# Kernel tuning notes

Measured on AMD Instinct MI355X. Metric: run time of the kernel, lower is better.

## Reference

```python
import jax, jax.numpy as jnp
import numpy as np

H, D = 4, 64          # n_heads, feats_per_head (hidden_size = H*D = 256)
NEG_SLOPE = 0.2       # DGL GATv2Conv default negative_slope

N_GT, N_UBS, N_AG = 100000, 20000, 20000
E_SEEN, E_NEAR = 320000, 160000
F_GT, F_UBS, F_AG = 8, 8, 16
HID = H * D


def _linear_params(key, fan_in, fan_out):
    kw, kb = jax.random.split(key)
    s = 1.0 / np.sqrt(fan_in)
    W = jax.random.uniform(kw, (fan_in, fan_out), jnp.float32, -s, s)
    b = jax.random.uniform(kb, (fan_out,), jnp.float32, -s, s)
    return W, b


def setup_inputs() -> dict:
    key = jax.random.key(0)
    ks = jax.random.split(key, 16)
    inp = {
        'x_gt': jax.random.normal(ks[0], (N_GT, F_GT), jnp.float32),
        'x_ubs': jax.random.normal(ks[1], (N_UBS, F_UBS), jnp.float32),
        'x_agent': jax.random.normal(ks[2], (N_AG, F_AG), jnp.float32),
        'seen_src': jax.random.randint(ks[3], (E_SEEN,), 0, N_GT, jnp.int32),
        'seen_dst': jax.random.randint(ks[4], (E_SEEN,), 0, N_AG, jnp.int32),
        'near_src': jax.random.randint(ks[5], (E_NEAR,), 0, N_UBS, jnp.int32),
        'near_dst': jax.random.randint(ks[6], (E_NEAR,), 0, N_AG, jnp.int32),
    }
    # GATv2Conv 'seen': (gt -> agent)
    inp['Ws_seen'], inp['bs_seen'] = _linear_params(ks[7], F_GT, HID)
    inp['Wd_seen'], inp['bd_seen'] = _linear_params(ks[8], F_AG, HID)
    inp['attn_seen'] = jax.random.normal(ks[9], (H, D), jnp.float32) * 0.1
    inp['Wr_seen'], inp['br_seen'] = _linear_params(ks[10], F_AG, HID)
    # GATv2Conv 'near': (ubs -> agent)
    inp['Ws_near'], inp['bs_near'] = _linear_params(ks[11], F_UBS, HID)
    inp['Wd_near'], inp['bd_near'] = _linear_params(ks[12], F_AG, HID)
    inp['attn_near'] = jax.random.normal(ks[13], (H, D), jnp.float32) * 0.1
    inp['Wr_near'], inp['br_near'] = _linear_params(ks[14], F_AG, HID)
    # aggregation MLP: Linear(2*HID, HID) + ReLU
    inp['W_aggr'], inp['b_aggr'] = _linear_params(ks[15], 2 * HID, HID)
    return inp


def _gatv2(h_src, h_dst, src, dst, Ws, bs, Wd, bd, attn, Wr, br, n_dst):
    # DGL GATv2Conv, bipartite, residual=True, allow_zero_in_degree, ReLU activation
    fs = (h_src @ Ws + bs).reshape(-1, H, D)   # [Ns,H,D]
    fd = (h_dst @ Wd + bd).reshape(-1, H, D)   # [Nd,H,D]
    e = jax.nn.leaky_relu(fs[src] + fd[dst], NEG_SLOPE)     # [E,H,D]
    scores = jnp.einsum('ehd,hd->eh', e, attn)              # [E,H]
    # edge softmax over incoming edges of each dst node
    m = jax.ops.segment_max(scores, dst, num_segments=n_dst)
    m = jnp.where(jnp.isfinite(m), m, 0.0)                  # zero-in-degree guard
    ex = jnp.exp(scores - m[dst])
    denom = jax.ops.segment_sum(ex, dst, num_segments=n_dst)
    alpha = ex / denom[dst]                                 # [E,H]
    rst = jax.ops.segment_sum(alpha[:, :, None] * fs[src], dst, num_segments=n_dst)
    rst = rst + (h_dst @ Wr + br).reshape(-1, H, D)         # residual
    return jax.nn.relu(rst).reshape(n_dst, H * D)


def reference(x_gt, x_ubs, x_agent, seen_src, seen_dst, near_src, near_dst,
              Ws_seen, bs_seen, Wd_seen, bd_seen, attn_seen, Wr_seen, br_seen,
              Ws_near, bs_near, Wd_near, bd_near, attn_near, Wr_near, br_near,
              W_aggr, b_aggr):
    n_ag = x_agent.shape[0]
    x1 = _gatv2(x_gt, x_agent, seen_src, seen_dst,
                Ws_seen, bs_seen, Wd_seen, bd_seen, attn_seen, Wr_seen, br_seen, n_ag)
    x2 = _gatv2(x_ubs, x_agent, near_src, near_dst,
                Ws_near, bs_near, Wd_near, bd_near, attn_near, Wr_near, br_near, n_ag)
    x_out = jnp.concatenate((x1, x2), axis=1)               # [N_ag, 2*HID]
    return jax.nn.relu(x_out @ W_aggr + b_aggr)             # [N_ag, HID]
```

## Files before the change

kernel.cpp:

```cpp
#include <hip/hip_runtime.h>
#include <math.h>

#define NEG 0.2f

typedef short bf16x8 __attribute__((ext_vector_type(8)));
typedef float f32x4  __attribute__((ext_vector_type(4)));
typedef float f32x2  __attribute__((ext_vector_type(2)));

static __device__ __forceinline__ void fma4(float4& d, float s, const float4 w) {
    d.x = fmaf(s, w.x, d.x); d.y = fmaf(s, w.y, d.y);
    d.z = fmaf(s, w.z, d.z); d.w = fmaf(s, w.w, d.w);
}
static __device__ __forceinline__ f32x2 pkfma(f32x2 a, f32x2 b, f32x2 c) {
    return __builtin_elementwise_fma(a, b, c);
}
static __device__ __forceinline__ f32x2 splat2(float x) { return (f32x2){x, x}; }

static __device__ __forceinline__ unsigned short f2bf(float f) {
    unsigned int x = __float_as_uint(f);
    unsigned int r = (x + 0x7FFFu + ((x >> 16) & 1u)) >> 16;
    return (unsigned short)r;
}
static __device__ __forceinline__ float rlane(float v, int l) {
    return __int_as_float(__builtin_amdgcn_readlane(__float_as_int(v), l));
}

#define DPP_ADD(x, ctrl) \
    ((x) + __int_as_float(__builtin_amdgcn_update_dpp( \
        __float_as_int(x), __float_as_int(x), (ctrl), 0xF, 0xF, true)))
static __device__ __forceinline__ float rowsum16(float v) {
    v = DPP_ADD(v, 0xB1);
    v = DPP_ADD(v, 0x4E);
    v = DPP_ADD(v, 0x141);
    v = DPP_ADD(v, 0x140);
    return v;
}

__global__ void k_hist_wt(const int* __restrict__ dst_s, int Es,
                          const int* __restrict__ dst_n, int En,
                          int* __restrict__ deg_s, int* __restrict__ deg_n,
                          const float* __restrict__ W, unsigned short* __restrict__ Wt) {
    int i = blockIdx.x * 256 + threadIdx.x;
    if (i < Es) atomicAdd(&deg_s[dst_s[i]], 1);
    int j = i - Es;
    if (j >= 0 && j < En) atomicAdd(&deg_n[dst_n[j]], 1);
    if (i < 512 * 256) {
        int k = i >> 8, n = i & 255;
        Wt[(size_t)n * 512 + k] = f2bf(W[i]);
    }
}

__global__ __launch_bounds__(1024) void k_scan2(int* a, int na, int* b, int nb) {
    int* p = (blockIdx.x == 0) ? a : b;
    int n  = (blockIdx.x == 0) ? na : nb;
    __shared__ int sums[1024];
    int t = threadIdx.x;
    int C = (n + 1023) >> 10;
    int base = t * C;
    int s = 0;
    for (int j = 0; j < C; ++j) { int i = base + j; if (i < n) s += p[i]; }
    sums[t] = s;
    __syncthreads();
    for (int off = 1; off < 1024; off <<= 1) {
        int v = (t >= off) ? sums[t - off] : 0;
        __syncthreads();
        sums[t] += v;
        __syncthreads();
    }
    int run = (t == 0) ? 0 : sums[t - 1];
    for (int j = 0; j < C; ++j) {
        int i = base + j;
        if (i < n) { int v = p[i]; p[i] = run; run += v; }
    }
}

__global__ void k_scatter(const int* __restrict__ src_s, const int* __restrict__ dst_s, int Es,
                          const int* __restrict__ src_n, const int* __restrict__ dst_n, int En,
                          int* __restrict__ cur_s, int* __restrict__ cur_n,
                          int* __restrict__ csr_s, int* __restrict__ csr_n) {
    int i = blockIdx.x * 256 + threadIdx.x;
    if (i < Es) {
        int pos = atomicAdd(&cur_s[dst_s[i]], 1);
        csr_s[pos] = src_s[i];
    }
    int j = i - Es;
    if (j >= 0 && j < En) {
        int pos = atomicAdd(&cur_n[dst_n[j]], 1);
        csr_n[pos] = src_n[j];
    }
}

__global__ __launch_bounds__(256) void k_gat(
    const float* __restrict__ xsrc_s, const int* __restrict__ pfx_s, const int* __restrict__ csr_s,
    const float* __restrict__ Ws_s, const float* __restrict__ bs_s,
    const float* __restrict__ Wd_s, const float* __restrict__ bd_s,
    const float* __restrict__ at_s,
    const float* __restrict__ Wr_s, const float* __restrict__ br_s,
    const float* __restrict__ xsrc_n, const int* __restrict__ pfx_n, const int* __restrict__ csr_n,
    const float* __restrict__ Ws_n, const float* __restrict__ bs_n,
    const float* __restrict__ Wd_n, const float* __restrict__ bd_n,
    const float* __restrict__ at_n,
    const float* __restrict__ Wr_n, const float* __restrict__ br_n,
    const float* __restrict__ x_ag,
    unsigned short* __restrict__ xcat, int n_dst, int gNs)
{
    const bool seen = (int)blockIdx.x < gNs;
    const float* x_src = seen ? xsrc_s : xsrc_n;
    const int*   pfx   = seen ? pfx_s  : pfx_n;
    const int*   csr   = seen ? csr_s  : csr_n;
    const float* Ws    = seen ? Ws_s   : Ws_n;
    const float* bs    = seen ? bs_s   : bs_n;
    const float* Wd    = seen ? Wd_s   : Wd_n;
    const float* bd    = seen ? bd_s   : bd_n;
    const float* at    = seen ? at_s   : at_n;
    const float* Wr    = seen ? Wr_s   : Wr_n;
    const float* br    = seen ? br_s   : br_n;
    const int col = seen ? 0 : 256;
    const int blk = seen ? (int)blockIdx.x : (int)blockIdx.x - gNs;

    const int t = threadIdx.x;
    const int wave = t >> 6, lane = t & 63;
    const int d0 = lane * 4;

    int gnode = blk * 16 + ((lane >> 4) << 2) + wave;
    int gn = (gnode < n_dst) ? gnode : (n_dst - 1);
    float xag = x_ag[(size_t)gn * 16 + (lane & 15)];

    int e_start[4], e_end[4];
#pragma unroll
    for (int j = 0; j < 4; ++j) {
        int nd = blk * 16 + j * 4 + wave;
        nd = (nd < n_dst) ? nd : (n_dst - 1);
        e_end[j]   = pfx[nd];
        e_start[j] = nd ? pfx[nd - 1] : 0;
    }

    f32x2 fd01[4], fd23[4], fr01[4], fr23[4];
    {
        float4 bdv = *(const float4*)&bd[d0];
        float4 brv = *(const float4*)&br[d0];
#pragma unroll
        for (int j = 0; j < 4; ++j) {
            fd01[j] = (f32x2){bdv.x, bdv.y}; fd23[j] = (f32x2){bdv.z, bdv.w};
            fr01[j] = (f32x2){brv.x, brv.y}; fr23[j] = (f32x2){brv.z, brv.w};
        }
#pragma unroll
        for (int k = 0; k < 16; ++k) {
            float4 wd = *(const float4*)&Wd[k * 256 + d0];
            float4 wr = *(const float4*)&Wr[k * 256 + d0];
            f32x2 wd01 = {wd.x, wd.y}, wd23 = {wd.z, wd.w};
            f32x2 wr01 = {wr.x, wr.y}, wr23 = {wr.z, wr.w};
#pragma unroll
            for (int j = 0; j < 4; ++j) {
                f32x2 xk = splat2(rlane(xag, j * 16 + k));
                fd01[j] = pkfma(xk, wd01, fd01[j]);
                fd23[j] = pkfma(xk, wd23, fd23[j]);
                fr01[j] = pkfma(xk, wr01, fr01[j]);
                fr23[j] = pkfma(xk, wr23, fr23[j]);
            }
        }
    }

    f32x2 ws01[8], ws23[8];
#pragma unroll
    for (int k = 0; k < 8; ++k) {
        float4 w = *(const float4*)&Ws[k * 256 + d0];
        ws01[k] = (f32x2){w.x, w.y};
        ws23[k] = (f32x2){w.z, w.w};
    }
    f32x2 bs01, bs23, at01, at23;
    {
        float4 b4 = *(const float4*)&bs[d0];
        float4 a4 = *(const float4*)&at[d0];
        bs01 = (f32x2){b4.x, b4.y}; bs23 = (f32x2){b4.z, b4.w};
        at01 = (f32x2){a4.x, a4.y}; at23 = (f32x2){a4.z, a4.w};
    }

#pragma unroll
    for (int rep = 0; rep < 4; ++rep) {
        const int node = blk * 16 + rep * 4 + wave;
        if (node >= n_dst) continue;

        const int start = e_start[rep];
        const int deg   = e_end[rep] - start;
        const f32x2 fd01r = fd01[rep], fd23r = fd23[rep];

        float l = 0.f;
        f32x2 a01 = {0.f, 0.f}, a23 = {0.f, 0.f};

        if (deg > 0) {
            const int gs = lane >> 3;
            const int w8 = lane & 7;

            int e0 = (gs < deg) ? gs : deg - 1;
            int i0 = csr[start + e0];
            float r0 = x_src[(size_t)i0 * 8 + w8];
            int e1 = (8 + gs < deg) ? 8 + gs : deg - 1;
            int i1 = csr[start + e1];

            for (int base = 0; base < deg; base += 8) {
                float r1 = x_src[(size_t)i1 * 8 + w8];
                int e2 = base + 16 + gs; e2 = (e2 < deg) ? e2 : deg - 1;
                int i2 = csr[start + e2];

#pragma unroll
                for (int j = 0; j < 8; ++j) {
                    if (base + j < deg) {
                        f32x2 x0 = splat2(rlane(r0, j * 8 + 0));
                        f32x2 x1 = splat2(rlane(r0, j * 8 + 1));
                        f32x2 x2 = splat2(rlane(r0, j * 8 + 2));
                        f32x2 x3 = splat2(rlane(r0, j * 8 + 3));
                        f32x2 x4 = splat2(rlane(r0, j * 8 + 4));
                        f32x2 x5 = splat2(rlane(r0, j * 8 + 5));
                        f32x2 x6 = splat2(rlane(r0, j * 8 + 6));
                        f32x2 x7 = splat2(rlane(r0, j * 8 + 7));

                        f32x2 fs01 = bs01, fs23 = bs23;
                        fs01 = pkfma(x0, ws01[0], fs01); fs23 = pkfma(x0, ws23[0], fs23);
                        fs01 = pkfma(x1, ws01[1], fs01); fs23 = pkfma(x1, ws23[1], fs23);
                        fs01 = pkfma(x2, ws01[2], fs01); fs23 = pkfma(x2, ws23[2], fs23);
                        fs01 = pkfma(x3, ws01[3], fs01); fs23 = pkfma(x3, ws23[3], fs23);
                        fs01 = pkfma(x4, ws01[4], fs01); fs23 = pkfma(x4, ws23[4], fs23);
                        fs01 = pkfma(x5, ws01[5], fs01); fs23 = pkfma(x5, ws23[5], fs23);
                        fs01 = pkfma(x6, ws01[6], fs01); fs23 = pkfma(x6, ws23[6], fs23);
                        fs01 = pkfma(x7, ws01[7], fs01); fs23 = pkfma(x7, ws23[7], fs23);

                        f32x2 t01 = fs01 + fd01r;
                        f32x2 t23 = fs23 + fd23r;
                        t01 = __builtin_elementwise_max(t01, NEG * t01);
                        t23 = __builtin_elementwise_max(t23, NEG * t23);

                        f32x2 scp = t01 * at01;
                        scp = pkfma(t23, at23, scp);
                        float sc = scp.x + scp.y;
                        sc = rowsum16(sc);

                        float p = __expf(sc);
                        l += p;
                        f32x2 pp = splat2(p);
                        a01 = pkfma(pp, fs01, a01);
                        a23 = pkfma(pp, fs23, a23);
                    }
                }
                r0 = r1; i1 = i2;
            }
        }

        float inv = (l > 0.f) ? 1.f / l : 0.f;
        ushort4 o;
        o.x = f2bf(fmaxf(fmaf(a01.x, inv, fr01[rep].x), 0.f));
        o.y = f2bf(fmaxf(fmaf(a01.y, inv, fr01[rep].y), 0.f));
        o.z = f2bf(fmaxf(fmaf(a23.x, inv, fr23[rep].x), 0.f));
        o.w = f2bf(fmaxf(fmaf(a23.y, inv, fr23[rep].y), 0.f));
        *(ushort4*)&xcat[(size_t)node * 512 + col + d0] = o;
    }
}

__global__ __launch_bounds__(256) void k_mlp(
    const unsigned short* __restrict__ X, const unsigned short* __restrict__ Wt,
    const float* __restrict__ b, float* __restrict__ out, int M)
{
    const int t = threadIdx.x;
    const int wave = t >> 6, lane = t & 63;
    const int m16 = lane & 15, q = lane >> 4;
    const int rbase = blockIdx.x * 16;
    const int nbase = wave * 64;

    int rowa = rbase + m16; if (rowa >= M) rowa = M - 1;
    const unsigned short* xp = X + (size_t)rowa * 512 + q * 8;
    const unsigned short* w0 = Wt + (size_t)(nbase + m16) * 512 + q * 8;
    const unsigned short* w1 = w0 + 16 * 512;
    const unsigned short* w2 = w0 + 32 * 512;
    const unsigned short* w3 = w0 + 48 * 512;

    f32x4 ac0 = {0.f, 0.f, 0.f, 0.f}, ac1 = ac0, ac2 = ac0, ac3 = ac0;

#pragma unroll
    for (int k0 = 0; k0 < 512; k0 += 32) {
        bf16x8 a  = *(const bf16x8*)(xp + k0);
        bf16x8 b0 = *(const bf16x8*)(w0 + k0);
        bf16x8 b1 = *(const bf16x8*)(w1 + k0);
        bf16x8 b2 = *(const bf16x8*)(w2 + k0);
        bf16x8 b3 = *(const bf16x8*)(w3 + k0);
        ac0 = __builtin_amdgcn_mfma_f32_16x16x32_bf16(a, b0, ac0, 0, 0, 0);
        ac1 = __builtin_amdgcn_mfma_f32_16x16x32_bf16(a, b1, ac1, 0, 0, 0);
        ac2 = __builtin_amdgcn_mfma_f32_16x16x32_bf16(a, b2, ac2, 0, 0, 0);
        ac3 = __builtin_amdgcn_mfma_f32_16x16x32_bf16(a, b3, ac3, 0, 0, 0);
    }

#define EPI(AC, J) { \
        int coln = nbase + (J) * 16 + m16; \
        float bias = b[coln]; \
        _Pragma("unroll") \
        for (int r = 0; r < 4; ++r) { \
            int orow = rbase + q * 4 + r; \
            if (orow < M) \
                out[(size_t)orow * 256 + coln] = fmaxf(AC[r] + bias, 0.f); \
        } }
    EPI(ac0, 0) EPI(ac1, 1) EPI(ac2, 2) EPI(ac3, 3)
#undef EPI
}

extern "C" void kernel_launch(void* const* d_in, const int* in_sizes, int n_in,
                              void* d_out, int out_size, void* d_ws, size_t ws_size,
                              hipStream_t stream) {
    const float* x_gt   = (const float*)d_in[0];
    const float* x_ubs  = (const float*)d_in[1];
    const float* x_ag   = (const float*)d_in[2];
    const int* seen_src = (const int*)d_in[3];
    const int* seen_dst = (const int*)d_in[4];
    const int* near_src = (const int*)d_in[5];
    const int* near_dst = (const int*)d_in[6];
    const float* Ws_s = (const float*)d_in[7];  const float* bs_s = (const float*)d_in[8];
    const float* Wd_s = (const float*)d_in[9];  const float* bd_s = (const float*)d_in[10];
    const float* at_s = (const float*)d_in[11];
    const float* Wr_s = (const float*)d_in[12]; const float* br_s = (const float*)d_in[13];
    const float* Ws_n = (const float*)d_in[14]; const float* bs_n = (const float*)d_in[15];
    const float* Wd_n = (const float*)d_in[16]; const float* bd_n = (const float*)d_in[17];
    const float* at_n = (const float*)d_in[18];
    const float* Wr_n = (const float*)d_in[19]; const float* br_n = (const float*)d_in[20];
    const float* W_a  = (const float*)d_in[21]; const float* b_a  = (const float*)d_in[22];

    const int n_ag = in_sizes[2] / 16;
    const int E_s  = in_sizes[3];
    const int E_n  = in_sizes[5];

    char* ws = (char*)d_ws;
    int* cur_s = (int*)ws;              ws += (size_t)n_ag * 4;
    int* cur_n = (int*)ws;              ws += (size_t)n_ag * 4;
    int* csr_s = (int*)ws;              ws += (size_t)E_s * 4;
    int* csr_n = (int*)ws;              ws += (size_t)E_n * 4;
    unsigned short* xcat = (unsigned short*)ws;  ws += (size_t)n_ag * 512 * 2;
    unsigned short* Wt   = (unsigned short*)ws;

    hipMemsetAsync(cur_s, 0, (size_t)n_ag * 8, stream);

    int gE = (E_s + E_n + 255) / 256;
    k_hist_wt<<<gE, 256, 0, stream>>>(seen_dst, E_s, near_dst, E_n, cur_s, cur_n, W_a, Wt);
    k_scan2<<<2, 1024, 0, stream>>>(cur_s, n_ag, cur_n, n_ag);
    k_scatter<<<gE, 256, 0, stream>>>(seen_src, seen_dst, E_s, near_src, near_dst, E_n,
                                      cur_s, cur_n, csr_s, csr_n);

    int gN = (n_ag + 15) / 16;
    k_gat<<<2 * gN, 256, 0, stream>>>(
        x_gt,  cur_s, csr_s, Ws_s, bs_s, Wd_s, bd_s, at_s, Wr_s, br_s,
        x_ubs, cur_n, csr_n, Ws_n, bs_n, Wd_n, bd_n, at_n, Wr_n, br_n,
        x_ag, xcat, n_ag, gN);

    k_mlp<<<(n_ag + 15) / 16, 256, 0, stream>>>(xcat, Wt, b_a, (float*)d_out, n_ag);
}
```

Baseline: 310.2 us.

## Fuse both GATv2 layers and the aggregation MLP into one kernel via shared memory

Merges the two-layer GAT kernel and the MLP kernel into a single kernel. Each block now handles both edge types for its 16 destination nodes in turn, writes the bf16 concatenated features into shared memory, and runs the MFMA GEMM directly from LDS. This removes the global xcat round trip and one kernel launch. In exchange the grid is halved (gN instead of 2*gN blocks), so each block does twice the serial gather work and there is less parallelism to hide latency.

Measured after the change: 347.1 us. 1.12x slower.

```diff
diff --git a/kernel.cpp b/kernel.cpp
--- a/kernel.cpp
+++ b/kernel.cpp
@@ -7,10 +7,6 @@
 typedef float f32x4  __attribute__((ext_vector_type(4)));
 typedef float f32x2  __attribute__((ext_vector_type(2)));
 
-static __device__ __forceinline__ void fma4(float4& d, float s, const float4 w) {
-    d.x = fmaf(s, w.x, d.x); d.y = fmaf(s, w.y, d.y);
-    d.z = fmaf(s, w.z, d.z); d.w = fmaf(s, w.w, d.w);
-}
 static __device__ __forceinline__ f32x2 pkfma(f32x2 a, f32x2 b, f32x2 c) {
     return __builtin_elementwise_fma(a, b, c);
 }
@@ -90,7 +86,7 @@
     }
 }
 
-__global__ __launch_bounds__(256) void k_gat(
+__global__ __launch_bounds__(256) void k_fused(
     const float* __restrict__ xsrc_s, const int* __restrict__ pfx_s, const int* __restrict__ csr_s,
     const float* __restrict__ Ws_s, const float* __restrict__ bs_s,
     const float* __restrict__ Wd_s, const float* __restrict__ bd_s,
@@ -102,203 +98,205 @@
     const float* __restrict__ at_n,
     const float* __restrict__ Wr_n, const float* __restrict__ br_n,
     const float* __restrict__ x_ag,
-    unsigned short* __restrict__ xcat, int n_dst, int gNs)
+    const unsigned short* __restrict__ Wt, const float* __restrict__ bias,
+    float* __restrict__ out, int n_dst)
 {
-    const bool seen = (int)blockIdx.x < gNs;
-    const float* x_src = seen ? xsrc_s : xsrc_n;
-    const int*   pfx   = seen ? pfx_s  : pfx_n;
-    const int*   csr   = seen ? csr_s  : csr_n;
-    const float* Ws    = seen ? Ws_s   : Ws_n;
-    const float* bs    = seen ? bs_s   : bs_n;
-    const float* Wd    = seen ? Wd_s   : Wd_n;
-    const float* bd    = seen ? bd_s   : bd_n;
-    const float* at    = seen ? at_s   : at_n;
-    const float* Wr    = seen ? Wr_s   : Wr_n;
-    const float* br    = seen ? br_s   : br_n;
-    const int col = seen ? 0 : 256;
-    const int blk = seen ? (int)blockIdx.x : (int)blockIdx.x - gNs;
-
+    __shared__ __align__(16) unsigned short sX[16][520];
+
+    const int blk = blockIdx.x;
     const int t = threadIdx.x;
     const int wave = t >> 6, lane = t & 63;
     const int d0 = lane * 4;
 
-    int gnode = blk * 16 + ((lane >> 4) << 2) + wave;
-    int gn = (gnode < n_dst) ? gnode : (n_dst - 1);
-    float xag = x_ag[(size_t)gn * 16 + (lane & 15)];
-
-    int e_start[4], e_end[4];
-#pragma unroll
-    for (int j = 0; j < 4; ++j) {
-        int nd = blk * 16 + j * 4 + wave;
-        nd = (nd < n_dst) ? nd : (n_dst - 1);
-        e_end[j]   = pfx[nd];
-        e_start[j] = nd ? pfx[nd - 1] : 0;
-    }
-
-    f32x2 fd01[4], fd23[4], fr01[4], fr23[4];
+#pragma unroll 1
+    for (int layer = 0; layer < 2; ++layer) {
+        const float* x_src = layer ? xsrc_n : xsrc_s;
+        const int*   pfx   = layer ? pfx_n  : pfx_s;
+        const int*   csr   = layer ? csr_n  : csr_s;
+        const float* Ws    = layer ? Ws_n   : Ws_s;
+        const float* bs    = layer ? bs_n   : bs_s;
+        const float* Wd    = layer ? Wd_n   : Wd_s;
+        const float* bd    = layer ? bd_n   : bd_s;
+        const float* at    = layer ? at_n   : at_s;
+        const float* Wr    = layer ? Wr_n   : Wr_s;
+        const float* br    = layer ? br_n   : br_s;
+        const int col = layer ? 256 : 0;
+
+        int gnode = blk * 16 + ((lane >> 4) << 2) + wave;
+        int gn = (gnode < n_dst) ? gnode : (n_dst - 1);
+        float xag = x_ag[(size_t)gn * 16 + (lane & 15)];
+
+        int e_start[4], e_end[4];
+#pragma unroll
+        for (int j = 0; j < 4; ++j) {
+            int nd = blk * 16 + j * 4 + wave;
+            nd = (nd < n_dst) ? nd : (n_dst - 1);
+            e_end[j]   = pfx[nd];
+            e_start[j] = nd ? pfx[nd - 1] : 0;
+        }
+
+        f32x2 fd01[4], fd23[4], fr01[4], fr23[4];
+        {
+            float4 bdv = *(const float4*)&bd[d0];
+            float4 brv = *(const float4*)&br[d0];
+#pragma unroll
+            for (int j = 0; j < 4; ++j) {
+                fd01[j] = (f32x2){bdv.x, bdv.y}; fd23[j] = (f32x2){bdv.z, bdv.w};
+                fr01[j] = (f32x2){brv.x, brv.y}; fr23[j] = (f32x2){brv.z, brv.w};
+            }
+#pragma unroll
+            for (int k = 0; k < 16; ++k) {
+                float4 wd = *(const float4*)&Wd[k * 256 + d0];
+                float4 wr = *(const float4*)&Wr[k * 256 + d0];
+                f32x2 wd01 = {wd.x, wd.y}, wd23 = {wd.z, wd.w};
+                f32x2 wr01 = {wr.x, wr.y}, wr23 = {wr.z, wr.w};
+#pragma unroll
+                for (int j = 0; j < 4; ++j) {
+                    f32x2 xk = splat2(rlane(xag, j * 16 + k));
+                    fd01[j] = pkfma(xk, wd01, fd01[j]);
+                    fd23[j] = pkfma(xk, wd23, fd23[j]);
+                    fr01[j] = pkfma(xk, wr01, fr01[j]);
+                    fr23[j] = pkfma(xk, wr23, fr23[j]);
+                }
+            }
+        }
+
+        f32x2 ws01[8], ws23[8];
+#pragma unroll
+        for (int k = 0; k < 8; ++k) {
+            float4 w = *(const float4*)&Ws[k * 256 + d0];
+            ws01[k] = (f32x2){w.x, w.y};
+            ws23[k] = (f32x2){w.z, w.w};
+        }
+        f32x2 bs01, bs23, at01, at23;
+        {
+            float4 b4 = *(const float4*)&bs[d0];
+            float4 a4 = *(const float4*)&at[d0];
+            bs01 = (f32x2){b4.x, b4.y}; bs23 = (f32x2){b4.z, b4.w};
+            at01 = (f32x2){a4.x, a4.y}; at23 = (f32x2){a4.z, a4.w};
+        }
+
+#pragma unroll
+        for (int rep = 0; rep < 4; ++rep) {
+            const int node = blk * 16 + rep * 4 + wave;
+            const int lrow = rep * 4 + wave;
+            if (node >= n_dst) continue;
+
+            const int start = e_start[rep];
+            const int deg   = e_end[rep] - start;
+            const f32x2 fd01r = fd01[rep], fd23r = fd23[rep];
+
+            float l = 0.f;
+            f32x2 a01 = {0.f, 0.f}, a23 = {0.f, 0.f};
+
+            if (deg > 0) {
+                const int gs = lane >> 3;
+                const int w8 = lane & 7;
+
+                int e0 = (gs < deg) ? gs : deg - 1;
+                int i0 = csr[start + e0];
+                float r0 = x_src[(size_t)i0 * 8 + w8];
+                int e1 = (8 + gs < deg) ? 8 + gs : deg - 1;
+                int i1 = csr[start + e1];
+
+                for (int base = 0; base < deg; base += 8) {
+                    float r1 = x_src[(size_t)i1 * 8 + w8];
+                    int e2 = base + 16 + gs; e2 = (e2 < deg) ? e2 : deg - 1;
+                    int i2 = csr[start + e2];
+
+#pragma unroll
+                    for (int j = 0; j < 8; ++j) {
+                        if (base + j < deg) {
+                            f32x2 x0 = splat2(rlane(r0, j * 8 + 0));
+                            f32x2 x1 = splat2(rlane(r0, j * 8 + 1));
+                            f32x2 x2 = splat2(rlane(r0, j * 8 + 2));
+                            f32x2 x3 = splat2(rlane(r0, j * 8 + 3));
+                            f32x2 x4 = splat2(rlane(r0, j * 8 + 4));
+                            f32x2 x5 = splat2(rlane(r0, j * 8 + 5));
+                            f32x2 x6 = splat2(rlane(r0, j * 8 + 6));
+                            f32x2 x7 = splat2(rlane(r0, j * 8 + 7));
+
+                            f32x2 fs01 = bs01, fs23 = bs23;
+                            fs01 = pkfma(x0, ws01[0], fs01); fs23 = pkfma(x0, ws23[0], fs23);
+                            fs01 = pkfma(x1, ws01[1], fs01); fs23 = pkfma(x1, ws23[1], fs23);
+                            fs01 = pkfma(x2, ws01[2], fs01); fs23 = pkfma(x2, ws23[2], fs23);
+                            fs01 = pkfma(x3, ws01[3], fs01); fs23 = pkfma(x3, ws23[3], fs23);
+                            fs01 = pkfma(x4, ws01[4], fs01); fs23 = pkfma(x4, ws23[4], fs23);
+                            fs01 = pkfma(x5, ws01[5], fs01); fs23 = pkfma(x5, ws23[5], fs23);
+                            fs01 = pkfma(x6, ws01[6], fs01); fs23 = pkfma(x6, ws23[6], fs23);
+                            fs01 = pkfma(x7, ws01[7], fs01); fs23 = pkfma(x7, ws23[7], fs23);
+
+                            f32x2 t01 = fs01 + fd01r;
+                            f32x2 t23 = fs23 + fd23r;
+                            t01 = __builtin_elementwise_max(t01, NEG * t01);
+                            t23 = __builtin_elementwise_max(t23, NEG * t23);
+
+                            f32x2 scp = t01 * at01;
+                            scp = pkfma(t23, at23, scp);
+                            float sc = scp.x + scp.y;
+                            sc = rowsum16(sc);
+
+                            float p = __expf(sc);
+                            l += p;
+                            f32x2 pp = splat2(p);
+                            a01 = pkfma(pp, fs01, a01);
+                            a23 = pkfma(pp, fs23, a23);
+                        }
+                    }
+                    r0 = r1; i1 = i2;
+                }
+            }
+
+            float inv = (l > 0.f) ? 1.f / l : 0.f;
+            ushort4 o;
+            o.x = f2bf(fmaxf(fmaf(a01.x, inv, fr01[rep].x), 0.f));
+            o.y = f2bf(fmaxf(fmaf(a01.y, inv, fr01[rep].y), 0.f));
+            o.z = f2bf(fmaxf(fmaf(a23.x, inv, fr23[rep].x), 0.f));
+            o.w = f2bf(fmaxf(fmaf(a23.y, inv, fr23[rep].y), 0.f));
+            *(ushort4*)&sX[lrow][col + d0] = o;
+        }
+    }
+
+    __syncthreads();
+
     {
-        float4 bdv = *(const float4*)&bd[d0];
-        float4 brv = *(const float4*)&br[d0];
-#pragma unroll
-        for (int j = 0; j < 4; ++j) {
-            fd01[j] = (f32x2){bdv.x, bdv.y}; fd23[j] = (f32x2){bdv.z, bdv.w};
-            fr01[j] = (f32x2){brv.x, brv.y}; fr23[j] = (f32x2){brv.z, brv.w};
-        }
-#pragma unroll
-        for (int k = 0; k < 16; ++k) {
-            float4 wd = *(const float4*)&Wd[k * 256 + d0];
-            float4 wr = *(const float4*)&Wr[k * 256 + d0];
-            f32x2 wd01 = {wd.x, wd.y}, wd23 = {wd.z, wd.w};
-            f32x2 wr01 = {wr.x, wr.y}, wr23 = {wr.z, wr.w};
-#pragma unroll
-            for (int j = 0; j < 4; ++j) {
-                f32x2 xk = splat2(rlane(xag, j * 16 + k));
-                fd01[j] = pkfma(xk, wd01, fd01[j]);
-                fd23[j] = pkfma(xk, wd23, fd23[j]);
-                fr01[j] = pkfma(xk, wr01, fr01[j]);
-                fr23[j] = pkfma(xk, wr23, fr23[j]);
-            }
-        }
-    }
-
-    f32x2 ws01[8], ws23[8];
-#pragma unroll
-    for (int k = 0; k < 8; ++k) {
-        float4 w = *(const float4*)&Ws[k * 256 + d0];
-        ws01[k] = (f32x2){w.x, w.y};
-        ws23[k] = (f32x2){w.z, w.w};
-    }
-    f32x2 bs01, bs23, at01, at23;
-    {
-        float4 b4 = *(const float4*)&bs[d0];
-        float4 a4 = *(const float4*)&at[d0];
-        bs01 = (f32x2){b4.x, b4.y}; bs23 = (f32x2){b4.z, b4.w};
-        at01 = (f32x2){a4.x, a4.y}; at23 = (f32x2){a4.z, a4.w};
-    }
-
-#pragma unroll
-    for (int rep = 0; rep < 4; ++rep) {
-        const int node = blk * 16 + rep * 4 + wave;
-        if (node >= n_dst) continue;
-
-        const int start = e_start[rep];
-        const int deg   = e_end[rep] - start;
-        const f32x2 fd01r = fd01[rep], fd23r = fd23[rep];
-
-        float l = 0.f;
-        f32x2 a01 = {0.f, 0.f}, a23 = {0.f, 0.f};
-
-        if (deg > 0) {
-            const int gs = lane >> 3;
-            const int w8 = lane & 7;
-
-            int e0 = (gs < deg) ? gs : deg - 1;
-            int i0 = csr[start + e0];
-            float r0 = x_src[(size_t)i0 * 8 + w8];
-            int e1 = (8 + gs < deg) ? 8 + gs : deg - 1;
-            int i1 = csr[start + e1];
-
-            for (int base = 0; base < deg; base += 8) {
-                float r1 = x_src[(size_t)i1 * 8 + w8];
-                int e2 = base + 16 + gs; e2 = (e2 < deg) ? e2 : deg - 1;
-                int i2 = csr[start + e2];
-
-#pragma unroll
-                for (int j = 0; j < 8; ++j) {
-                    if (base + j < deg) {
-                        f32x2 x0 = splat2(rlane(r0, j * 8 + 0));
-                        f32x2 x1 = splat2(rlane(r0, j * 8 + 1));
-                        f32x2 x2 = splat2(rlane(r0, j * 8 + 2));
-                        f32x2 x3 = splat2(rlane(r0, j * 8 + 3));
-                        f32x2 x4 = splat2(rlane(r0, j * 8 + 4));
-                        f32x2 x5 = splat2(rlane(r0, j * 8 + 5));
-                        f32x2 x6 = splat2(rlane(r0, j * 8 + 6));
-                        f32x2 x7 = splat2(rlane(r0, j * 8 + 7));
-
-                        f32x2 fs01 = bs01, fs23 = bs23;
-                        fs01 = pkfma(x0, ws01[0], fs01); fs23 = pkfma(x0, ws23[0], fs23);
-                        fs01 = pkfma(x1, ws01[1], fs01); fs23 = pkfma(x1, ws23[1], fs23);
-                        fs01 = pkfma(x2, ws01[2], fs01); fs23 = pkfma(x2, ws23[2], fs23);
-                        fs01 = pkfma(x3, ws01[3], fs01); fs23 = pkfma(x3, ws23[3], fs23);
-                        fs01 = pkfma(x4, ws01[4], fs01); fs23 = pkfma(x4, ws23[4], fs23);
-                        fs01 = pkfma(x5, ws01[5], fs01); fs23 = pkfma(x5, ws23[5], fs23);
-                        fs01 = pkfma(x6, ws01[6], fs01); fs23 = pkfma(x6, ws23[6], fs23);
-                        fs01 = pkfma(x7, ws01[7], fs01); fs23 = pkfma(x7, ws23[7], fs23);
-
-                        f32x2 t01 = fs01 + fd01r;
-                        f32x2 t23 = fs23 + fd23r;
-                        t01 = __builtin_elementwise_max(t01, NEG * t01);
-                        t23 = __builtin_elementwise_max(t23, NEG * t23);
-
-                        f32x2 scp = t01 * at01;
-                        scp = pkfma(t23, at23, scp);
-                        float sc = scp.x + scp.y;
-                        sc = rowsum16(sc);
-
-                        float p = __expf(sc);
-                        l += p;
-                        f32x2 pp = splat2(p);
-                        a01 = pkfma(pp, fs01, a01);
-                        a23 = pkfma(pp, fs23, a23);
-                    }
-                }
-                r0 = r1; i1 = i2;
-            }
-        }
-
-        float inv = (l > 0.f) ? 1.f / l : 0.f;
-        ushort4 o;
-        o.x = f2bf(fmaxf(fmaf(a01.x, inv, fr01[rep].x), 0.f));
-        o.y = f2bf(fmaxf(fmaf(a01.y, inv, fr01[rep].y), 0.f));
-        o.z = f2bf(fmaxf(fmaf(a23.x, inv, fr23[rep].x), 0.f));
-        o.w = f2bf(fmaxf(fmaf(a23.y, inv, fr23[rep].y), 0.f));
-        *(ushort4*)&xcat[(size_t)node * 512 + col + d0] = o;
-    }
-}
-
-__global__ __launch_bounds__(256) void k_mlp(
-    const unsigned short* __restrict__ X, const unsigned short* __restrict__ Wt,
-    const float* __restrict__ b, float* __restrict__ out, int M)
-{
-    const int t = threadIdx.x;
-    const int wave = t >> 6, lane = t & 63;
-    const int m16 = lane & 15, q = lane >> 4;
-    const int rbase = blockIdx.x * 16;
-    const int nbase = wave * 64;
-
-    int rowa = rbase + m16; if (rowa >= M) rowa = M - 1;
-    const unsigned short* xp = X + (size_t)rowa * 512 + q * 8;
-    const unsigned short* w0 = Wt + (size_t)(nbase + m16) * 512 + q * 8;
-    const unsigned short* w1 = w0 + 16 * 512;
-    const unsigned short* w2 = w0 + 32 * 512;
-    const unsigned short* w3 = w0 + 48 * 512;
-
-    f32x4 ac0 = {0.f, 0.f, 0.f, 0.f}, ac1 = ac0, ac2 = ac0, ac3 = ac0;
-
-#pragma unroll
-    for (int k0 = 0; k0 < 512; k0 += 32) {
-        bf16x8 a  = *(const bf16x8*)(xp + k0);
-        bf16x8 b0 = *(const bf16x8*)(w0 + k0);
-        bf16x8 b1 = *(const bf16x8*)(w1 + k0);
-        bf16x8 b2 = *(const bf16x8*)(w2 + k0);
-        bf16x8 b3 = *(const bf16x8*)(w3 + k0);
-        ac0 = __builtin_amdgcn_mfma_f32_16x16x32_bf16(a, b0, ac0, 0, 0, 0);
-        ac1 = __builtin_amdgcn_mfma_f32_16x16x32_bf16(a, b1, ac1, 0, 0, 0);
-        ac2 = __builtin_amdgcn_mfma_f32_16x16x32_bf16(a, b2, ac2, 0, 0, 0);
-        ac3 = __builtin_amdgcn_mfma_f32_16x16x32_bf16(a, b3, ac3, 0, 0, 0);
-    }
+        const int m16 = lane & 15, q = lane >> 4;
+        const int rbase = blk * 16;
+        const int nbase = wave * 64;
+
+        const unsigned short* w0 = Wt + (size_t)(nbase + m16) * 512 + q * 8;
+        const unsigned short* w1 = w0 + 16 * 512;
+        const unsigned short* w2 = w0 + 32 * 512;
+        const unsigned short* w3 = w0 + 48 * 512;
+        const unsigned short* xp = &sX[m16][q * 8];
+
+        f32x4 ac0 = {0.f, 0.f, 0.f, 0.f}, ac1 = ac0, ac2 = ac0, ac3 = ac0;
+
+#pragma unroll
+        for (int k0 = 0; k0 < 512; k0 += 32) {
+            bf16x8 a  = *(const bf16x8*)(xp + k0);
+            bf16x8 b0 = *(const bf16x8*)(w0 + k0);
+            bf16x8 b1 = *(const bf16x8*)(w1 + k0);
+            bf16x8 b2 = *(const bf16x8*)(w2 + k0);
+            bf16x8 b3 = *(const bf16x8*)(w3 + k0);
+            ac0 = __builtin_amdgcn_mfma_f32_16x16x32_bf16(a, b0, ac0, 0, 0, 0);
+            ac1 = __builtin_amdgcn_mfma_f32_16x16x32_bf16(a, b1, ac1, 0, 0, 0);
+            ac2 = __builtin_amdgcn_mfma_f32_16x16x32_bf16(a, b2, ac2, 0, 0, 0);
+            ac3 = __builtin_amdgcn_mfma_f32_16x16x32_bf16(a, b3, ac3, 0, 0, 0);
+        }
 
 #define EPI(AC, J) { \
-        int coln = nbase + (J) * 16 + m16; \
-        float bias = b[coln]; \
-        _Pragma("unroll") \
-        for (int r = 0; r < 4; ++r) { \
-            int orow = rbase + q * 4 + r; \
-            if (orow < M) \
-                out[(size_t)orow * 256 + coln] = fmaxf(AC[r] + bias, 0.f); \
-        } }
-    EPI(ac0, 0) EPI(ac1, 1) EPI(ac2, 2) EPI(ac3, 3)
+            int coln = nbase + (J) * 16 + m16; \
+            float bv = bias[coln]; \
+            _Pragma("unroll") \
+            for (int r = 0; r < 4; ++r) { \
+                int orow = rbase + q * 4 + r; \
+                if (orow < n_dst) \
+                    out[(size_t)orow * 256 + coln] = fmaxf(AC[r] + bv, 0.f); \
+            } }
+        EPI(ac0, 0) EPI(ac1, 1) EPI(ac2, 2) EPI(ac3, 3)
 #undef EPI
+    }
 }
 
 extern "C" void kernel_launch(void* const* d_in, const int* in_sizes, int n_in,
@@ -330,8 +328,7 @@
     int* cur_n = (int*)ws;              ws += (size_t)n_ag * 4;
     int* csr_s = (int*)ws;              ws += (size_t)E_s * 4;
     int* csr_n = (int*)ws;              ws += (size_t)E_n * 4;
-    unsigned short* xcat = (unsigned short*)ws;  ws += (size_t)n_ag * 512 * 2;
-    unsigned short* Wt   = (unsigned short*)ws;
+    unsigned short* Wt = (unsigned short*)ws;
 
     hipMemsetAsync(cur_s, 0, (size_t)n_ag * 8, stream);
 
@@ -342,10 +339,8 @@
                                       cur_s, cur_n, csr_s, csr_n);
 
     int gN = (n_ag + 15) / 16;
-    k_gat<<<2 * gN, 256, 0, stream>>>(
+    k_fused<<<gN, 256, 0, stream>>>(
         x_gt,  cur_s, csr_s, Ws_s, bs_s, Wd_s, bd_s, at_s, Wr_s, br_s,
         x_ubs, cur_n, csr_n, Ws_n, bs_n, Wd_n, bd_n, at_n, Wr_n, br_n,
-        x_ag, xcat, n_ag, gN);
-
-    k_mlp<<<(n_ag + 15) / 16, 256, 0, stream>>>(xcat, Wt, b_a, (float*)d_out, n_ag);
-}
+        x_ag, Wt, b_a, (float*)d_out, n_ag);
+}
```
